# Performance work log

Measured on AMD Instinct MI355X. Metric: run time of the kernel, lower is better.

The kernel has to match this reference:

```python
import jax, jax.numpy as jnp
import numpy as np

T, B, I, H = 32, 8, 512, 512
CLIP = 1.0


def _softshrink(x, lambd=0.5):
    return jnp.where(x > lambd, x - lambd, jnp.where(x < -lambd, x + lambd, jnp.zeros_like(x)))


def setup_inputs() -> dict:
    key = jax.random.key(0)
    ks = jax.random.split(key, 5)
    sc = lambda k, sh, s: (s * jax.random.normal(k, sh)).astype(jnp.float32)
    return {
        "x": jax.random.normal(ks[0], (T, B, I), dtype=jnp.float32),
        "h0": jnp.zeros((B, H), jnp.float32),
        "v0": jnp.zeros((B, H), jnp.float32),
        "dU0": jnp.zeros((B, H, H), jnp.float32),
        "trace_e0": jnp.zeros((B, H), jnp.float32),
        "trace_E0": jnp.zeros((B, H, H), jnp.float32),
        "x2h_v": sc(ks[1], (3 * H, I), 0.05),
        "x2h_g": jnp.ones((3 * H,), jnp.float32),
        "x2h_b": jnp.zeros((3 * H,), jnp.float32),
        "h2h_v": sc(ks[2], (3 * H, H), 0.05),
        "h2h_g": jnp.ones((3 * H,), jnp.float32),
        "h2h_b": jnp.zeros((3 * H,), jnp.float32).at[:H].set(-1.0),
        "alpha": 0.1 * jnp.ones((1, H, H), jnp.float32),
        "h2mod_w": sc(ks[3], (4, H), 0.05),
        "h2mod_b": jnp.array([0.0, -2.0, -2.0, -3.0], jnp.float32),
        "modU_w": jnp.ones((1, H, H), jnp.float32),
        "modU_b": jnp.zeros((1, H, H), jnp.float32),
    }


def reference(x, h0, v0, dU0, trace_e0, trace_E0, x2h_v, x2h_g, x2h_b,
              h2h_v, h2h_g, h2h_b, alpha, h2mod_w, h2mod_b, modU_w, modU_b):
    Hd = h0.shape[-1]
    # weight_norm (dim=0): w[i,:] = g[i] * v[i,:] / ||v[i,:]||
    wn = lambda vv, g: g[:, None] * vv / jnp.linalg.norm(vv, axis=1, keepdims=True)
    Wx = wn(x2h_v, x2h_g)          # [3H, I]
    Wh = wn(h2h_v, h2h_g)          # [3H, H]
    # input projections for all timesteps at once
    xproj = jnp.einsum('tbi,oi->tbo', x, Wx) + x2h_b   # [T, B, 3H]
    Wr = Wh[Hd:2 * Hd]             # h2h.weight rows for r-gate, used in the dU clamp
    up = jax.nn.relu(CLIP - Wr) / (alpha + 1e-5)        # [1, H, H]
    lo = -jax.nn.relu(CLIP + Wr) / (alpha + 1e-5)       # [1, H, H]

    def step(carry, xp):
        h, v, dU, te, tE = carry
        hp = h @ Wh.T + h2h_b
        zx, rx, dvx = jnp.split(xp, 3, axis=-1)
        zh, rh, dvh = jnp.split(hp, 3, axis=-1)
        z = jax.nn.sigmoid(zx + zh)
        # NOTE: r = sigmoid(rx + rh) is computed in the original but never used in the update.
        dv = dvx + dvh + jnp.einsum('bij,bj->bi', alpha * dU, h)
        v_n = (1.0 - z) * v + z * dv
        hn = jax.nn.relu(v_n)                            # activation == 'relu'
        mod = hn @ h2mod_w.T + h2mod_b                   # [B, 4]
        tau_e = jax.nn.sigmoid(mod[:, 0:1])              # [B, 1]
        tau_E = jax.nn.sigmoid(mod[:, 1:2])[:, :, None]  # [B, 1, 1]
        tau_U = jax.nn.sigmoid(mod[:, 2:3])[:, :, None]  # [B, 1, 1]
        mU = jax.nn.relu(mod[:, 3:4])[:, :, None]        # [B, 1, 1]
        te_n = (1.0 - tau_e) * te + tau_e * h            # uses OLD h
        outer = hn[:, :, None] * te_n[:, None, :] - te_n[:, :, None] * hn[:, None, :]
        tE_n = (1.0 - tau_E) * tE + tau_E * outer
        dU_n = (1.0 - tau_U) * dU + tau_U * _softshrink(mU * modU_w + modU_b) * tE_n
        dU_n = jnp.clip(dU_n, lo, up)
        return (hn, v_n, dU_n, te_n, tE_n), hn

    (h, v, dU, te, tE), outs = jax.lax.scan(step, (h0, v0, dU0, trace_e0, trace_E0), xproj)
    return v, h, dU, te, tE, outs
```

## Files before the change

### kernel.cpp

```cpp
#include <hip/hip_runtime.h>
#include <math.h>


#define ATOMIC_LD(p) __hip_atomic_load((p), __ATOMIC_RELAXED, __HIP_MEMORY_SCOPE_AGENT)
#define ATOMIC_ST(p, v) __hip_atomic_store((p), (v), __ATOMIC_RELAXED, __HIP_MEMORY_SCOPE_AGENT)

__device__ __forceinline__ float wred(float v) {
#pragma unroll
  for (int o = 32; o > 0; o >>= 1) v += __shfl_xor(v, o, 64);
  return v;
}
__device__ __forceinline__ float sigm(float x) { return 1.f / (1.f + __expf(-x)); }

__global__ void prenorm_kernel(const float* __restrict__ xv, const float* __restrict__ xg,
                               const float* __restrict__ hv, const float* __restrict__ hg,
                               float* __restrict__ scx, float* __restrict__ sch,
                               unsigned* __restrict__ exch) {
  int r = blockIdx.x, L = threadIdx.x;
  if (r < 2048) exch[r * 64 + L] = 0u;
  const float* vrow; const float* g; float* o; int rr;
  if (r < 1536) { rr = r; vrow = xv + (size_t)r * 512; g = xg; o = scx; }
  else { rr = r - 1536; vrow = hv + (size_t)rr * 512; g = hg; o = sch; }
  float s = 0.f;
#pragma unroll
  for (int m = 0; m < 8; m++) { float v = vrow[m * 64 + L]; s = fmaf(v, v, s); }
  s = wred(s);
  if (L == 0) o[rr] = g[rr] / sqrtf(s);
}

__global__ __launch_bounds__(1024, 4) void persist_kernel(
    const float* __restrict__ x,
    const float* __restrict__ h0, const float* __restrict__ v0,
    const float* __restrict__ dU0, const float* __restrict__ te0,
    const float* __restrict__ tE0,
    const float* __restrict__ x2h_v, const float* __restrict__ x2h_b,
    const float* __restrict__ h2h_v, const float* __restrict__ h2h_b,
    const float* __restrict__ alpha,
    const float* __restrict__ h2mod_w, const float* __restrict__ h2mod_b,
    const float* __restrict__ modU_w, const float* __restrict__ modU_b,
    const float* __restrict__ scx, const float* __restrict__ sch,
    unsigned* __restrict__ exch,
    float* __restrict__ o_v, float* __restrict__ o_h,
    float* __restrict__ o_dU, float* __restrict__ o_te,
    float* __restrict__ o_tE, float* __restrict__ o_outs) {
  __shared__ float sh_hbuf[2][512];
  __shared__ float sh_te[512];
  __shared__ float sh_mod[2048];
  __shared__ float sh_xpz[32][16];
  __shared__ float sh_xpdv[32][16];
  __shared__ float sh_gates[4];
  __shared__ float sh_gather[16];

  const int tid = threadIdx.x;
  const int w = tid >> 6, L = tid & 63;
  const int b = blockIdx.x & 7, q = blockIdx.x >> 3;
  const int i = q * 16 + w;

  if (tid < 512) {
    sh_hbuf[0][tid] = h0[b * 512 + tid];
    sh_te[tid] = te0[b * 512 + tid];
  }
  sh_mod[tid] = h2mod_w[tid];
  sh_mod[tid + 1024] = h2mod_w[tid + 1024];

  const int rz = i, rdv = 1024 + i, rr = 512 + i;
  const size_t row  = ((size_t)(b * 512 + i)) * 512;
  const size_t wrow = (size_t)i * 512;

  {
    float xz[8], xdv[8];
    const float sx_z = scx[rz], sx_dv = scx[rdv];
#pragma unroll
    for (int m = 0; m < 8; m++) {
      int c = m * 64 + L;
      xz[m]  = sx_z  * x2h_v[(size_t)rz  * 512 + c];
      xdv[m] = sx_dv * x2h_v[(size_t)rdv * 512 + c];
    }
    float bz = 0.f, bdv = 0.f;
    if (L == 0) {
      bz  = x2h_b[i] + h2h_b[i];
      bdv = x2h_b[1024 + i] + h2h_b[1024 + i];
    }
#pragma unroll 4
    for (int t = 0; t < 32; t++) {
      const float* xr = x + (size_t)t * 4096 + b * 512;
      float a = 0.f, d = 0.f;
#pragma unroll
      for (int m = 0; m < 8; m++) {
        int c = m * 64 + L;
        float xv_ = xr[c];
        a = fmaf(xz[m], xv_, a);
        d = fmaf(xdv[m], xv_, d);
      }
      a = wred(a); d = wred(d);
      if (L == 0) { sh_xpz[t][w] = a + bz; sh_xpdv[t][w] = d + bdv; }
    }
  }

  float wz[8], wdv[8], mw[8], mb[8], al[8], upS[8], loS[8], D[8], tE[8];
  {
    const float s_z = sch[rz], s_dv = sch[rdv], s_r = sch[rr];
#pragma unroll
    for (int m = 0; m < 8; m++) {
      int c = m * 64 + L;
      wz[m]  = s_z  * h2h_v[(size_t)rz  * 512 + c];
      wdv[m] = s_dv * h2h_v[(size_t)rdv * 512 + c];
      mw[m] = modU_w[wrow + c];
      mb[m] = modU_b[wrow + c];
      float alv = alpha[wrow + c];
      al[m] = alv;
      float wrv = s_r * h2h_v[(size_t)rr * 512 + c];
      float t1 = alv / (alv + 1e-5f);
      upS[m] = fmaxf(1.f - wrv, 0.f) * t1;
      loS[m] = -fmaxf(1.f + wrv, 0.f) * t1;
      float dui = dU0[row + c];
      D[m]  = alv * dui;
      tE[m] = tE0[row + c];
    }
  }
  float v_reg = 0.f, hn_last = 0.f, gb = 0.f;
  if (L == 0) {
    v_reg = v0[b * 512 + i];
    if (w < 4) gb = h2mod_b[w];
  }
  __syncthreads();

  for (int t = 0; t <= 32; t++) {
    const int cur = t & 1, prev = cur ^ 1;
    if (t > 0) {
      const unsigned* eb = exch + ((t - 1) * 8 + b) * 512;
      if (w == 0) {
        const unsigned* fp = eb + (L & 31) * 16 + (L & 15);
        unsigned u;
        do {
          u = ATOMIC_LD(fp);
        } while (!__all(u >> 31));
      }
      __syncthreads();
      if (tid < 512) {
        unsigned u = ATOMIC_LD(eb + tid);
        while (!(u >> 31)) u = ATOMIC_LD(eb + tid);
        sh_hbuf[cur][tid] = __uint_as_float(u & 0x7fffffffu);
      }
      __syncthreads();
      if (w < 4) {
        float p = 0.f;
        const float* mr = sh_mod + w * 512;
#pragma unroll
        for (int m = 0; m < 8; m++) {
          int c = m * 64 + L;
          p = fmaf(sh_hbuf[cur][c], mr[c], p);
        }
        p = wred(p);
        if (L == 0) {
          p += gb;
          sh_gates[w] = (w == 3) ? fmaxf(p, 0.f) : sigm(p);
        }
      }
      __syncthreads();
      float taue = sh_gates[0];
      if (tid < 512) sh_te[tid] += taue * (sh_hbuf[prev][tid] - sh_te[tid]);
      __syncthreads();
      float tauE = sh_gates[1], tauU = sh_gates[2], mU = sh_gates[3];
      float hn_i = sh_hbuf[cur][i], te_i = sh_te[i];
#pragma unroll
      for (int m = 0; m < 8; m++) {
        int j = m * 64 + L;
        float outer = hn_i * sh_te[j] - te_i * sh_hbuf[cur][j];
        float tEn = tE[m] + tauE * (outer - tE[m]);
        float a = fmaf(mU, mw[m], mb[m]);
        float sshr = (a > 0.5f) ? (a - 0.5f) : ((a < -0.5f) ? (a + 0.5f) : 0.f);
        float Dn = D[m] + tauU * (sshr * (al[m] * tEn) - D[m]);
        D[m] = fminf(fmaxf(Dn, loS[m]), upS[m]);
        tE[m] = tEn;
      }
    }

    if (t < 32) {
      float p1 = 0.f, p2 = 0.f;
#pragma unroll
      for (int m = 0; m < 8; m++) {
        int c = m * 64 + L;
        float hc = sh_hbuf[cur][c];
        p1 = fmaf(wz[m], hc, p1);
        p2 = fmaf(wdv[m] + D[m], hc, p2);
      }
      p1 = wred(p1); p2 = wred(p2);
      if (L == 0) {
        float z = sigm(p1 + sh_xpz[t][w]);
        float dv = p2 + sh_xpdv[t][w];
        v_reg += z * (dv - v_reg);
        hn_last = fmaxf(v_reg, 0.f);
        o_outs[(size_t)t * 4096 + b * 512 + i] = hn_last;
        sh_gather[w] = hn_last;
      }
      __syncthreads();
      if (w == 15 && L < 16) {
        unsigned u = __float_as_uint(sh_gather[L]) | 0x80000000u;
        ATOMIC_ST(exch + (t * 8 + b) * 512 + q * 16 + L, u);
      }
    }
  }

#pragma unroll
  for (int m = 0; m < 8; m++) {
    int c = m * 64 + L;
    float alv = al[m];
    o_dU[row + c] = (alv != 0.f) ? D[m] * __builtin_amdgcn_rcpf(alv) : 0.f;
    o_tE[row + c] = tE[m];
  }
  if (L == 0) {
    o_v[b * 512 + i] = v_reg;
    o_h[b * 512 + i] = hn_last;
  }
  if (q == 0 && tid < 512) o_te[b * 512 + tid] = sh_te[tid];
}

extern "C" void kernel_launch(void* const* d_in, const int* in_sizes, int n_in,
                              void* d_out, int out_size, void* d_ws, size_t ws_size,
                              hipStream_t stream) {
  const float* x       = (const float*)d_in[0];
  const float* h0      = (const float*)d_in[1];
  const float* v0      = (const float*)d_in[2];
  const float* dU0     = (const float*)d_in[3];
  const float* te0     = (const float*)d_in[4];
  const float* tE0     = (const float*)d_in[5];
  const float* x2h_v   = (const float*)d_in[6];
  const float* x2h_g   = (const float*)d_in[7];
  const float* x2h_b   = (const float*)d_in[8];
  const float* h2h_v   = (const float*)d_in[9];
  const float* h2h_g   = (const float*)d_in[10];
  const float* h2h_b   = (const float*)d_in[11];
  const float* alpha   = (const float*)d_in[12];
  const float* h2mod_w = (const float*)d_in[13];
  const float* h2mod_b = (const float*)d_in[14];
  const float* modU_w  = (const float*)d_in[15];
  const float* modU_b  = (const float*)d_in[16];

  float* out = (float*)d_out;
  float* o_v    = out;
  float* o_h    = out + 4096;
  float* o_dU   = out + 8192;
  float* o_te   = out + 2105344;
  float* o_tE   = out + 2109440;
  float* o_outs = out + 4206592;

  float* wsf = (float*)d_ws;
  float* scx = wsf + 8192;
  float* sch = wsf + 9728;
  unsigned* exch = (unsigned*)d_ws + 12288;

  prenorm_kernel<<<dim3(3072), dim3(64), 0, stream>>>(x2h_v, x2h_g, h2h_v, h2h_g,
                                                      scx, sch, exch);

  persist_kernel<<<dim3(256), dim3(1024), 0, stream>>>(
      x, h0, v0, dU0, te0, tE0, x2h_v, x2h_b, h2h_v, h2h_b, alpha,
      h2mod_w, h2mod_b, modU_w, modU_b, scx, sch, exch,
      o_v, o_h, o_dU, o_te, o_tE, o_outs);
}
```

Baseline: 246.5 us.

## Spread exchange polling across all waves and double-buffer trace to drop barriers

The flag wait for the cross-block hidden-state exchange is now split over all 16 waves, each polling and loading its own 32-entry slice, instead of wave 0 polling and then a barrier. The eligibility trace te is double-buffered and recomputed redundantly inside the outer-product loop, with one wave per slice writing the new values. Together these remove two __syncthreads per timestep from the serial recurrence. The cost is extra shared-memory reads, redundant FMAs and more LDS use. The final te output reads buffer 0, which is correct only if the last step (t=32) wrote to buffer cur=0.

Result: slower. 286.3 us (+16.2%).

```diff
diff --git a/kernel.cpp b/kernel.cpp
--- a/kernel.cpp
+++ b/kernel.cpp
@@ -44,7 +44,7 @@
     float* __restrict__ o_dU, float* __restrict__ o_te,
     float* __restrict__ o_tE, float* __restrict__ o_outs) {
   __shared__ float sh_hbuf[2][512];
-  __shared__ float sh_te[512];
+  __shared__ float sh_te[2][512];
   __shared__ float sh_mod[2048];
   __shared__ float sh_xpz[32][16];
   __shared__ float sh_xpdv[32][16];
@@ -58,7 +58,7 @@
 
   if (tid < 512) {
     sh_hbuf[0][tid] = h0[b * 512 + tid];
-    sh_te[tid] = te0[b * 512 + tid];
+    sh_te[0][tid] = te0[b * 512 + tid];
   }
   sh_mod[tid] = h2mod_w[tid];
   sh_mod[tid + 1024] = h2mod_w[tid + 1024];
@@ -129,18 +129,15 @@
     const int cur = t & 1, prev = cur ^ 1;
     if (t > 0) {
       const unsigned* eb = exch + ((t - 1) * 8 + b) * 512;
-      if (w == 0) {
-        const unsigned* fp = eb + (L & 31) * 16 + (L & 15);
+      {
+        const unsigned* fp = eb + ((w * 2 + (L & 1)) << 4);
         unsigned u;
-        do {
-          u = ATOMIC_LD(fp);
-        } while (!__all(u >> 31));
-      }
-      __syncthreads();
-      if (tid < 512) {
-        unsigned u = ATOMIC_LD(eb + tid);
-        while (!(u >> 31)) u = ATOMIC_LD(eb + tid);
-        sh_hbuf[cur][tid] = __uint_as_float(u & 0x7fffffffu);
+        do { u = ATOMIC_LD(fp); } while (!__all(u >> 31));
+      }
+      if (L < 32) {
+        unsigned u = ATOMIC_LD(eb + w * 32 + L);
+        while (!(u >> 31)) u = ATOMIC_LD(eb + w * 32 + L);
+        sh_hbuf[cur][w * 32 + L] = __uint_as_float(u & 0x7fffffffu);
       }
       __syncthreads();
       if (w < 4) {
@@ -159,14 +156,17 @@
       }
       __syncthreads();
       float taue = sh_gates[0];
-      if (tid < 512) sh_te[tid] += taue * (sh_hbuf[prev][tid] - sh_te[tid]);
-      __syncthreads();
       float tauE = sh_gates[1], tauU = sh_gates[2], mU = sh_gates[3];
-      float hn_i = sh_hbuf[cur][i], te_i = sh_te[i];
+      float hn_i = sh_hbuf[cur][i];
+      float te_i = sh_te[prev][i];
+      te_i = fmaf(taue, sh_hbuf[prev][i] - te_i, te_i);
 #pragma unroll
       for (int m = 0; m < 8; m++) {
         int j = m * 64 + L;
-        float outer = hn_i * sh_te[j] - te_i * sh_hbuf[cur][j];
+        float tej = sh_te[prev][j];
+        float te_new = fmaf(taue, sh_hbuf[prev][j] - tej, tej);
+        if (m == w) sh_te[cur][j] = te_new;
+        float outer = hn_i * te_new - te_i * sh_hbuf[cur][j];
         float tEn = tE[m] + tauE * (outer - tE[m]);
         float a = fmaf(mU, mw[m], mb[m]);
         float sshr = (a > 0.5f) ? (a - 0.5f) : ((a < -0.5f) ? (a + 0.5f) : 0.f);
@@ -213,7 +213,7 @@
     o_v[b * 512 + i] = v_reg;
     o_h[b * 512 + i] = hn_last;
   }
-  if (q == 0 && tid < 512) o_te[b * 512 + tid] = sh_te[tid];
+  if (q == 0 && tid < 512) o_te[b * 512 + tid] = sh_te[0][tid];
 }
 
 extern "C" void kernel_launch(void* const* d_in, const int* in_sizes, int n_in,
```
